# Performance work log

Hardware: AMD Instinct MI355X
Metric: run time of the kernel (lower is better)

## Reference

```python
import jax, jax.numpy as jnp
import numpy as np

B = 2097152
ANGLE_WEIGHT = 100.0
EPS = 1e-07


def setup_inputs() -> dict:
    key = jax.random.key(0)
    k1, k2 = jax.random.split(key)
    predictions = jax.random.normal(k1, (B, 6), dtype=jnp.float32)
    targets = jax.random.normal(k2, (B, 6), dtype=jnp.float32)
    return {"predictions": predictions, "targets": targets}


def _euler_xyz_to_matrix(e):
    # scipy Rotation.from_euler('xyz', [a,b,c]) (lowercase = extrinsic):
    # R = Rz(c) @ Ry(b) @ Rx(a)
    a, b, c = e[:, 0], e[:, 1], e[:, 2]
    ca, sa = jnp.cos(a), jnp.sin(a)
    cb, sb = jnp.cos(b), jnp.sin(b)
    cc, sc = jnp.cos(c), jnp.sin(c)
    r00 = cb * cc
    r01 = cc * sa * sb - ca * sc
    r02 = sc * sa + ca * cc * sb
    r10 = cb * sc
    r11 = ca * cc + sa * sb * sc
    r12 = ca * sb * sc - cc * sa
    r20 = -sb
    r21 = cb * sa
    r22 = ca * cb
    return jnp.stack([
        jnp.stack([r00, r01, r02], axis=-1),
        jnp.stack([r10, r11, r12], axis=-1),
        jnp.stack([r20, r21, r22], axis=-1),
    ], axis=-2)  # [B, 3, 3]


def _smooth_l1(pred, tgt):
    # torch smooth_l1_loss, beta=1.0, reduction='mean'
    d = pred - tgt
    ad = jnp.abs(d)
    per = jnp.where(ad < 1.0, 0.5 * d * d, ad - 0.5)
    return jnp.mean(per)


def reference(predictions, targets):
    trans_loss = _smooth_l1(predictions[:, :3], targets[:, :3])
    pred_mat = _euler_xyz_to_matrix(predictions[:, 3:])
    gt_mat = _euler_xyz_to_matrix(targets[:, 3:])
    # trace(gt^T @ pred) == sum(gt * pred) elementwise — avoids the bmm
    trace = jnp.sum(gt_mat * pred_mat, axis=(1, 2))
    cos_angle = jnp.clip((trace - 1.0) * 0.5, -1.0 + EPS, 1.0 - EPS)
    rot_loss = jnp.mean(jnp.arccos(cos_angle))
    return trans_loss + ANGLE_WEIGHT * rot_loss
```

## Files before the change

kernel.cpp:

```cpp
#include <hip/hip_runtime.h>


constexpr int   B_ROWS  = 2097152;
constexpr int   NBLK    = 2048;
constexpr int   TPB     = 256;
constexpr int   NTHREAD = NBLK * TPB;
constexpr float ANGLE_WEIGHT = 100.0f;
constexpr float EPS_F        = 1e-7f;

typedef float f32x4 __attribute__((ext_vector_type(4)));

__device__ inline float smooth_l1_term(float d) {
    float ad = fabsf(d);
    return ad < 1.0f ? 0.5f * d * d : ad - 0.5f;
}

__device__ inline void euler_xyz_mat(float a, float b, float c, float r[9]) {
    float sa, ca, sb, cb, sc, cc;
    __sincosf(a, &sa, &ca);
    __sincosf(b, &sb, &cb);
    __sincosf(c, &sc, &cc);
    r[0] = cb * cc;
    r[1] = cc * sa * sb - ca * sc;
    r[2] = sc * sa + ca * cc * sb;
    r[3] = cb * sc;
    r[4] = ca * cc + sa * sb * sc;
    r[5] = ca * sb * sc - cc * sa;
    r[6] = -sb;
    r[7] = cb * sa;
    r[8] = ca * cb;
}

__device__ inline void accum_row(float px, float py, float pz,
                                 float pa, float pb, float pc,
                                 float tx, float ty, float tz,
                                 float ta, float tb, float tc,
                                 float& trans_acc, float& rot_acc) {
    trans_acc += smooth_l1_term(px - tx) + smooth_l1_term(py - ty) + smooth_l1_term(pz - tz);
    float rp[9], rt[9];
    euler_xyz_mat(pa, pb, pc, rp);
    euler_xyz_mat(ta, tb, tc, rt);
    float tr = 0.0f;
#pragma unroll
    for (int i = 0; i < 9; ++i) tr = fmaf(rp[i], rt[i], tr);
    float cosang = fminf(fmaxf((tr - 1.0f) * 0.5f, -1.0f + EPS_F), 1.0f - EPS_F);
    rot_acc += acosf(cosang);
}

__global__ __launch_bounds__(TPB, 4) void rpmg_partial_kernel(const float* __restrict__ pred,
                                                              const float* __restrict__ tgt,
                                                              float2* __restrict__ partial) {
    const int tid = blockIdx.x * TPB + threadIdx.x;
    const f32x4* pp1 = reinterpret_cast<const f32x4*>(pred) + (size_t)tid * 3;
    const f32x4* tp1 = reinterpret_cast<const f32x4*>(tgt)  + (size_t)tid * 3;
    const f32x4* pp2 = pp1 + (size_t)NTHREAD * 3;
    const f32x4* tp2 = tp1 + (size_t)NTHREAD * 3;

    f32x4 a0 = pp1[0], a1 = pp1[1], a2 = pp1[2];
    f32x4 b0 = tp1[0], b1 = tp1[1], b2 = tp1[2];
    f32x4 c0 = pp2[0], c1 = pp2[1], c2 = pp2[2];
    f32x4 d0 = tp2[0], d1 = tp2[1], d2 = tp2[2];

    float trans_acc = 0.0f, rot_acc = 0.0f;
    accum_row(a0[0], a0[1], a0[2], a0[3], a1[0], a1[1],
              b0[0], b0[1], b0[2], b0[3], b1[0], b1[1], trans_acc, rot_acc);
    accum_row(a1[2], a1[3], a2[0], a2[1], a2[2], a2[3],
              b1[2], b1[3], b2[0], b2[1], b2[2], b2[3], trans_acc, rot_acc);
    accum_row(c0[0], c0[1], c0[2], c0[3], c1[0], c1[1],
              d0[0], d0[1], d0[2], d0[3], d1[0], d1[1], trans_acc, rot_acc);
    accum_row(c1[2], c1[3], c2[0], c2[1], c2[2], c2[3],
              d1[2], d1[3], d2[0], d2[1], d2[2], d2[3], trans_acc, rot_acc);

#pragma unroll
    for (int off = 32; off > 0; off >>= 1) {
        trans_acc += __shfl_down(trans_acc, off, 64);
        rot_acc   += __shfl_down(rot_acc,   off, 64);
    }
    __shared__ float sa[TPB / 64], sb[TPB / 64];
    const int wid  = threadIdx.x >> 6;
    const int lane = threadIdx.x & 63;
    if (lane == 0) { sa[wid] = trans_acc; sb[wid] = rot_acc; }
    __syncthreads();
    if (threadIdx.x == 0) {
        float ta = 0.0f, tb = 0.0f;
#pragma unroll
        for (int w = 0; w < TPB / 64; ++w) { ta += sa[w]; tb += sb[w]; }
        partial[blockIdx.x] = make_float2(ta, tb);
    }
}

__global__ __launch_bounds__(TPB) void rpmg_final_kernel(const float2* __restrict__ partial,
                                                         float* __restrict__ out) {
    float ta = 0.0f, tb = 0.0f;
    for (int i = threadIdx.x; i < NBLK; i += TPB) {
        float2 v = partial[i];
        ta += v.x;
        tb += v.y;
    }
#pragma unroll
    for (int off = 32; off > 0; off >>= 1) {
        ta += __shfl_down(ta, off, 64);
        tb += __shfl_down(tb, off, 64);
    }
    __shared__ float sa[TPB / 64], sb[TPB / 64];
    const int wid  = threadIdx.x >> 6;
    const int lane = threadIdx.x & 63;
    if (lane == 0) { sa[wid] = ta; sb[wid] = tb; }
    __syncthreads();
    if (threadIdx.x == 0) {
        float st = 0.0f, sr = 0.0f;
#pragma unroll
        for (int w = 0; w < TPB / 64; ++w) { st += sa[w]; sr += sb[w]; }
        out[0] = st / (3.0f * (float)B_ROWS) + ANGLE_WEIGHT * (sr / (float)B_ROWS);
    }
}

extern "C" void kernel_launch(void* const* d_in, const int* in_sizes, int n_in,
                              void* d_out, int out_size, void* d_ws, size_t ws_size,
                              hipStream_t stream) {
    const float* pred = (const float*)d_in[0];
    const float* tgt  = (const float*)d_in[1];
    float* out        = (float*)d_out;
    float2* partial   = (float2*)d_ws;

    rpmg_partial_kernel<<<NBLK, TPB, 0, stream>>>(pred, tgt, partial);
    rpmg_final_kernel<<<1, TPB, 0, stream>>>(partial, out);
}
```

Baseline: 24.32 us.

## Stage row tiles through LDS for coalesced loads, two rows per thread

Each block now cooperatively loads a contiguous tile of predictions and targets into shared memory with fully coalesced 16-byte loads. Each thread then reads its own 3 vectors (two rows) from LDS instead of striding through global memory. The grid is doubled to 4096 blocks with two rows per thread instead of four, and the final reduction reads partials as float4. This adds an LDS round trip and a block barrier, and LDS reads at stride 3 may cause bank conflicts.

```diff
diff --git a/kernel.cpp b/kernel.cpp
--- a/kernel.cpp
+++ b/kernel.cpp
@@ -2,9 +2,9 @@
 
 
 constexpr int   B_ROWS  = 2097152;
-constexpr int   NBLK    = 2048;
 constexpr int   TPB     = 256;
-constexpr int   NTHREAD = NBLK * TPB;
+constexpr int   NBLK    = 4096;
+constexpr int   PAIRS_PER_BLK = TPB;
 constexpr float ANGLE_WEIGHT = 100.0f;
 constexpr float EPS_F        = 1e-7f;
 
@@ -47,29 +47,31 @@
     rot_acc += acosf(cosang);
 }
 
-__global__ __launch_bounds__(TPB, 4) void rpmg_partial_kernel(const float* __restrict__ pred,
-                                                              const float* __restrict__ tgt,
-                                                              float2* __restrict__ partial) {
-    const int tid = blockIdx.x * TPB + threadIdx.x;
-    const f32x4* pp1 = reinterpret_cast<const f32x4*>(pred) + (size_t)tid * 3;
-    const f32x4* tp1 = reinterpret_cast<const f32x4*>(tgt)  + (size_t)tid * 3;
-    const f32x4* pp2 = pp1 + (size_t)NTHREAD * 3;
-    const f32x4* tp2 = tp1 + (size_t)NTHREAD * 3;
+__global__ __launch_bounds__(TPB) void rpmg_partial_kernel(const float* __restrict__ pred,
+                                                           const float* __restrict__ tgt,
+                                                           float2* __restrict__ partial) {
+    __shared__ f32x4 ldsA[3 * TPB];
+    __shared__ f32x4 ldsB[3 * TPB];
 
-    f32x4 a0 = pp1[0], a1 = pp1[1], a2 = pp1[2];
-    f32x4 b0 = tp1[0], b1 = tp1[1], b2 = tp1[2];
-    f32x4 c0 = pp2[0], c1 = pp2[1], c2 = pp2[2];
-    f32x4 d0 = tp2[0], d1 = tp2[1], d2 = tp2[2];
+    const int t = threadIdx.x;
+    const size_t tile_x4 = (size_t)blockIdx.x * (3 * TPB);
+    const f32x4* pbase = reinterpret_cast<const f32x4*>(pred) + tile_x4;
+    const f32x4* tbase = reinterpret_cast<const f32x4*>(tgt)  + tile_x4;
+
+#pragma unroll
+    for (int k = 0; k < 3; ++k) ldsA[k * TPB + t] = pbase[k * TPB + t];
+#pragma unroll
+    for (int k = 0; k < 3; ++k) ldsB[k * TPB + t] = tbase[k * TPB + t];
+    __syncthreads();
+
+    f32x4 a0 = ldsA[t * 3 + 0], a1 = ldsA[t * 3 + 1], a2 = ldsA[t * 3 + 2];
+    f32x4 b0 = ldsB[t * 3 + 0], b1 = ldsB[t * 3 + 1], b2 = ldsB[t * 3 + 2];
 
     float trans_acc = 0.0f, rot_acc = 0.0f;
     accum_row(a0[0], a0[1], a0[2], a0[3], a1[0], a1[1],
               b0[0], b0[1], b0[2], b0[3], b1[0], b1[1], trans_acc, rot_acc);
     accum_row(a1[2], a1[3], a2[0], a2[1], a2[2], a2[3],
               b1[2], b1[3], b2[0], b2[1], b2[2], b2[3], trans_acc, rot_acc);
-    accum_row(c0[0], c0[1], c0[2], c0[3], c1[0], c1[1],
-              d0[0], d0[1], d0[2], d0[3], d1[0], d1[1], trans_acc, rot_acc);
-    accum_row(c1[2], c1[3], c2[0], c2[1], c2[2], c2[3],
-              d1[2], d1[3], d2[0], d2[1], d2[2], d2[3], trans_acc, rot_acc);
 
 #pragma unroll
     for (int off = 32; off > 0; off >>= 1) {
@@ -91,11 +93,12 @@
 
 __global__ __launch_bounds__(TPB) void rpmg_final_kernel(const float2* __restrict__ partial,
                                                          float* __restrict__ out) {
+    const float4* p4 = reinterpret_cast<const float4*>(partial);
     float ta = 0.0f, tb = 0.0f;
-    for (int i = threadIdx.x; i < NBLK; i += TPB) {
-        float2 v = partial[i];
-        ta += v.x;
-        tb += v.y;
+    for (int i = threadIdx.x; i < NBLK / 2; i += TPB) {
+        float4 v = p4[i];
+        ta += v.x + v.z;
+        tb += v.y + v.w;
     }
 #pragma unroll
     for (int off = 32; off > 0; off >>= 1) {
```

Result: no change. 24.46 us (+0.6%).
